# Performance work log

Hardware: AMD Instinct MI355X
Metric: run time of the kernel (lower is better)

## Reference

```python
import jax, jax.numpy as jnp
import numpy as np

EPS = 1e-07
B, C, NCON, NCC = 500000, 30, 8, 3
NH = 7  # hidden width


def _coarse_code():
    # [C, NCC] Gaussian bump coarse code, as built in __init__
    sigma = 0.25
    const_1 = 1.0 / (sigma * np.sqrt(6.28))
    ii = jnp.arange(C, dtype=jnp.float32)[:, None] / (C - 1)
    jj = jnp.arange(NCC, dtype=jnp.float32)[None, :] / (NCC - 1)
    return (const_1 * jnp.exp(-0.5 * jnp.square((ii - jj) / sigma))).astype(jnp.float32)


def _mlp(x, W1, b1, Wh, bh, Wo, bo):
    # x: [B, C, n_in]; six 7-unit ReLU layers then linear output (dropout inactive)
    h = jax.nn.relu(jnp.einsum('bci,hi->bch', x, W1) + b1)
    for i in range(Wh.shape[0]):
        h = jax.nn.relu(jnp.einsum('bci,hi->bch', h, Wh[i]) + bh[i])
    return jnp.einsum('bci,oi->bco', h, Wo) + bo


def setup_inputs() -> dict:
    key = jax.random.key(0)
    ks = jax.random.split(key, 16)
    u = lambda k, shape, lo, hi: jax.random.uniform(k, shape, jnp.float32, lo, hi)
    inp = {
        'tau': jax.random.uniform(ks[0], (B, C, NCON), jnp.float32),
        'mu_direct': jax.random.uniform(ks[1], (B, 1), jnp.float32),
        'mu_diffuse': jax.random.uniform(ks[2], (B, 1), jnp.float32),
        # net_direct: n_input = 5 + NCC + 1 = 9
        'Wd1': u(ks[3], (NH, 5 + NCC + 1), -1.0, 1.0),
        'bd1': u(ks[4], (NH,), 0.9, 1.1),
        'Wdh': u(ks[5], (5, NH, NH), -1.0, 1.0),
        'bdh': u(ks[6], (5, NH), 0.9, 1.1),
        'Wdo': u(ks[7], (3, NH), -1.0, 1.0),
        'bdo': u(ks[8], (3,), -0.1, 0.1),
        # net_diffuse: n_input = 5 + NCC = 8
        'Wf1': u(ks[9], (NH, 5 + NCC), -1.0, 1.0),
        'bf1': u(ks[10], (NH,), 0.9, 1.1),
        'Wfh': u(ks[11], (5, NH, NH), -1.0, 1.0),
        'bfh': u(ks[12], (5, NH), 0.9, 1.1),
        'Wfo': u(ks[13], (3, NH), -1.0, 1.0),
        'bfo': u(ks[14], (3,), -0.1, 0.1),
    }
    return inp


def reference(tau, mu_direct, mu_diffuse, Wd1, bd1, Wdh, bdh, Wdo, bdo,
              Wf1, bf1, Wfh, bfh, Wfo, bfo):
    tau_total = jnp.sum(tau, axis=2)                      # [B, C]
    t_direct = jnp.exp(-tau_total / (mu_direct + EPS))    # [B, C]
    t_diffuse = jnp.exp(-tau_total / (mu_diffuse + EPS))  # [B, C]

    mu_d = mu_direct[:, :, None]                          # [B, 1, 1]
    tau_direct = tau / (mu_d + EPS)                       # [B, C, NCON]

    direct_1 = (tau_direct[:, :, 3] + tau_direct[:, :, 4]
                + tau_direct[:, :, 6] + tau_direct[:, :, 7])[:, :, None]
    mu_rep = jnp.broadcast_to(mu_d, (tau.shape[0], C, 1))
    cc = jnp.broadcast_to(_coarse_code()[None], (tau.shape[0], C, NCC))

    direct = jnp.concatenate([tau_direct[:, :, 0:2], tau_direct[:, :, 5:6],
                              tau_direct[:, :, 2:3], direct_1, mu_rep, cc], axis=2)  # [B,C,9]

    diffuse_1 = (tau[:, :, 3] + tau[:, :, 4] + tau[:, :, 6] + tau[:, :, 7])[:, :, None]
    diffuse = jnp.concatenate([tau[:, :, 0:2], tau[:, :, 5:6],
                               tau[:, :, 2:3], diffuse_1, cc], axis=2)  # [B,C,8]

    e_split_direct = jax.nn.softmax(_mlp(direct, Wd1, bd1, Wdh, bdh, Wdo, bdo), axis=-1)
    e_split_diffuse = jax.nn.softmax(_mlp(diffuse, Wf1, bf1, Wfh, bfh, Wfo, bfo), axis=-1)
    return (t_direct, t_diffuse, e_split_direct, e_split_diffuse)
```

## Files before the change

### kernel.cpp

```cpp
#include <hip/hip_runtime.h>


#define B_SZ 500000
#define C_SZ 30
#define BC   (B_SZ * C_SZ)
#define EPSF 1e-7f
#define LOG2E 1.4426950408889634f

typedef float f2 __attribute__((ext_vector_type(2)));

enum {
    WD1P  = 0,
    WDHP  = 48,
    WDOP  = 328,
    BDOP  = 356,
    BEFFD = 360,
    BEFFF = 600,
    WF1P  = 840,
    WFHP  = 904,
    WFOP  = 1184,
    BFOP  = 1212,
    BDHP  = 1216,
    BFHP  = 1256,
    WS_FLOATS = 1296
};
#define FLAG_BYTE_OFF 6144

__device__ __forceinline__ float bf2f(unsigned short u) {
    union { unsigned int i; float f; } v;
    v.i = ((unsigned int)u) << 16;
    return v.f;
}

__device__ __forceinline__ unsigned short f2bf(float f) {
    union { float f; unsigned int i; } v;
    v.f = f;
    unsigned int u = v.i;
    unsigned int r = u + 0x7fffu + ((u >> 16) & 1u);
    return (unsigned short)(r >> 16);
}

__device__ __forceinline__ float ex2(float x) {
    float r;
    asm("v_exp_f32 %0, %1" : "=v"(r) : "v"(x));
    return r;
}

__device__ __forceinline__ unsigned int pk_bf16(float lo, float hi) {
    unsigned int r;
    asm("v_cvt_pk_bf16_f32 %0, %1, %2" : "=v"(r) : "v"(lo), "v"(hi));
    return r;
}

__device__ __forceinline__ f2 pkfma(f2 a, f2 b, f2 c) {
#if __has_builtin(__builtin_elementwise_fma)
    return __builtin_elementwise_fma(a, b, c);
#else
    f2 r; r.x = fmaf(a.x, b.x, c.x); r.y = fmaf(a.y, b.y, c.y); return r;
#endif
}

__device__ __forceinline__ f2 pkmax0(f2 a) {
    f2 z = {0.0f, 0.0f};
#if __has_builtin(__builtin_elementwise_max)
    return __builtin_elementwise_max(a, z);
#else
    f2 r; r.x = fmaxf(a.x, 0.f); r.y = fmaxf(a.y, 0.f); return r;
#endif
}

__device__ __forceinline__ f2 bc(f2 v, int hl) {
    return hl ? __builtin_shufflevector(v, v, 1, 1)
              : __builtin_shufflevector(v, v, 0, 0);
}

template <int NIN, int W1, int WH, int BH, int WO, int BO>
__device__ __forceinline__ void mlp_pk(const float* __restrict__ ws,
                                       const f2* __restrict__ x2,
                                       const f2* __restrict__ be,
                                       float* __restrict__ o) {
    const f2* w1 = (const f2*)(ws + W1);
    f2 h[4] = {be[0], be[1], be[2], be[3]};
#pragma unroll
    for (int i = 0; i < NIN; ++i) {
        f2 xx = bc(x2[i >> 1], i & 1);
#pragma unroll
        for (int p = 0; p < 4; ++p) h[p] = pkfma(xx, w1[i * 4 + p], h[p]);
    }
#pragma unroll
    for (int p = 0; p < 4; ++p) h[p] = pkmax0(h[p]);

    const f2* wh = (const f2*)(ws + WH);
    const f2* bh = (const f2*)(ws + BH);
#pragma unroll
    for (int l = 0; l < 5; ++l) {
        f2 hn[4];
#pragma unroll
        for (int p = 0; p < 4; ++p) hn[p] = bh[l * 4 + p];
#pragma unroll
        for (int i = 0; i < 7; ++i) {
            f2 xx = bc(h[i >> 1], i & 1);
#pragma unroll
            for (int p = 0; p < 4; ++p) hn[p] = pkfma(xx, wh[(l * 7 + i) * 4 + p], hn[p]);
        }
#pragma unroll
        for (int p = 0; p < 4; ++p) h[p] = pkmax0(hn[p]);
    }

    const f2* wo = (const f2*)(ws + WO);
    const f2* bo = (const f2*)(ws + BO);
    f2 oA = bo[0], oB = bo[1];
#pragma unroll
    for (int i = 0; i < 7; ++i) {
        f2 xx = bc(h[i >> 1], i & 1);
        oA = pkfma(xx, wo[i * 2 + 0], oA);
        oB = pkfma(xx, wo[i * 2 + 1], oB);
    }
    o[0] = oA.x; o[1] = oA.y; o[2] = oB.x;
}

struct P12 { const void* p[12]; };

__global__ void prep(P12 ptrs, const unsigned int* __restrict__ tau_raw,
                     float* __restrict__ ws, int* __restrict__ flagp)
{
    __shared__ int sflag;
    int tid = threadIdx.x;
    if (tid < 64) {
        unsigned long long m = __ballot((tau_raw[tid] & 0x8000u) != 0u);
        if (tid == 0) { sflag = (m != 0ull) ? 1 : 0; *flagp = sflag; }
    }
    __syncthreads();
    const int f32m = sflag;

    auto rd = [&](int seg, int idx) -> float {
        if (f32m) return ((const float*)ptrs.p[seg])[idx];
        return bf2f(((const unsigned short*)ptrs.p[seg])[idx]);
    };
    auto ccf = [&](int c, int k) -> float {
        const float C1 = 1.0f / (0.25f * sqrtf(6.28f));
        float ii = (float)c * (1.0f / 29.0f);
        float jj = (float)k * 0.5f;
        float d = (ii - jj) * 4.0f;
        return C1 * expf(-0.5f * d * d);
    };

    for (int i = tid; i < 48; i += 256) {
        int ii = i >> 3, p = (i >> 1) & 3, hl = i & 1, j = 2 * p + hl;
        ws[WD1P + i] = (j < 7) ? rd(0, j * 9 + ii) : 0.f;
    }
    for (int i = tid; i < 280; i += 256) {
        int l = i / 56, r = i % 56;
        int ii = r >> 3, p = (r >> 1) & 3, hl = r & 1, j = 2 * p + hl;
        ws[WDHP + i] = (j < 7) ? rd(2, l * 49 + j * 7 + ii) : 0.f;
    }
    for (int i = tid; i < 40; i += 256) {
        int l = i / 8, p = (i >> 1) & 3, hl = i & 1, j = 2 * p + hl;
        ws[BDHP + i] = (j < 7) ? rd(3, l * 7 + j) : 0.f;
    }
    for (int i = tid; i < 28; i += 256) {
        int ii = i >> 2, p = (i >> 1) & 1, hl = i & 1, k = 2 * p + hl;
        ws[WDOP + i] = (k < 3) ? rd(4, k * 7 + ii) * LOG2E : 0.f;
    }
    for (int i = tid; i < 4; i += 256)
        ws[BDOP + i] = (i < 3) ? rd(5, i) * LOG2E : 0.f;

    for (int i = tid; i < 240; i += 256) {
        int c = i / 8, j = i % 8; float v = 0.f;
        if (j < 7) v = rd(1, j) + rd(0, j * 9 + 6) * ccf(c, 0)
                               + rd(0, j * 9 + 7) * ccf(c, 1)
                               + rd(0, j * 9 + 8) * ccf(c, 2);
        ws[BEFFD + i] = v;
    }
    for (int i = tid; i < 240; i += 256) {
        int c = i / 8, j = i % 8; float v = 0.f;
        if (j < 7) v = rd(7, j) + rd(6, j * 8 + 5) * ccf(c, 0)
                               + rd(6, j * 8 + 6) * ccf(c, 1)
                               + rd(6, j * 8 + 7) * ccf(c, 2);
        ws[BEFFF + i] = v;
    }
    for (int i = tid; i < 64; i += 256) {
        int ii = i >> 3, p = (i >> 1) & 3, hl = i & 1, j = 2 * p + hl;
        const int cols[8] = {0, 1, 3, 4, 4, 2, 4, 4};
        ws[WF1P + i] = (j < 7) ? rd(6, j * 8 + cols[ii]) : 0.f;
    }
    for (int i = tid; i < 280; i += 256) {
        int l = i / 56, r = i % 56;
        int ii = r >> 3, p = (r >> 1) & 3, hl = r & 1, j = 2 * p + hl;
        ws[WFHP + i] = (j < 7) ? rd(8, l * 49 + j * 7 + ii) : 0.f;
    }
    for (int i = tid; i < 40; i += 256) {
        int l = i / 8, p = (i >> 1) & 3, hl = i & 1, j = 2 * p + hl;
        ws[BFHP + i] = (j < 7) ? rd(9, l * 7 + j) : 0.f;
    }
    for (int i = tid; i < 28; i += 256) {
        int ii = i >> 2, p = (i >> 1) & 1, hl = i & 1, k = 2 * p + hl;
        ws[WFOP + i] = (k < 3) ? rd(10, k * 7 + ii) * LOG2E : 0.f;
    }
    for (int i = tid; i < 4; i += 256)
        ws[BFOP + i] = (i < 3) ? rd(11, i) * LOG2E : 0.f;
}

__global__ __launch_bounds__(256) void scatter_main(
    const void* __restrict__ tau_p,
    const void* __restrict__ mu_dir_p,
    const void* __restrict__ mu_dif_p,
    const float* __restrict__ ws,
    const int* __restrict__ flag,
    void* __restrict__ out_p)
{
    __shared__ unsigned short sm[2048];

    int tid = threadIdx.x;
    int eb0 = blockIdx.x * 256;
    int e = eb0 + tid;
    bool act = (e < BC);
    int eL = act ? e : (BC - 1);
    int b = eL / C_SZ;
    int c = eL - b * C_SZ;
    bool tail = (eb0 + 256 > BC);

    int is_f32 = *flag;

    float t0, t1, t2, t3, t4, t5, t6, t7, mu_d, mu_f;
    if (is_f32) {
        const float4* tf = (const float4*)tau_p;
        float4 a = tf[2 * eL];
        float4 bq = tf[2 * eL + 1];
        t0 = a.x; t1 = a.y; t2 = a.z; t3 = a.w;
        t4 = bq.x; t5 = bq.y; t6 = bq.z; t7 = bq.w;
        mu_d = ((const float*)mu_dir_p)[b];
        mu_f = ((const float*)mu_dif_p)[b];
    } else {
        uint4 t = ((const uint4*)tau_p)[eL];
        t0 = bf2f((unsigned short)(t.x & 0xffffu));
        t1 = bf2f((unsigned short)(t.x >> 16));
        t2 = bf2f((unsigned short)(t.y & 0xffffu));
        t3 = bf2f((unsigned short)(t.y >> 16));
        t4 = bf2f((unsigned short)(t.z & 0xffffu));
        t5 = bf2f((unsigned short)(t.z >> 16));
        t6 = bf2f((unsigned short)(t.w & 0xffffu));
        t7 = bf2f((unsigned short)(t.w >> 16));
        mu_d = bf2f(((const unsigned short*)mu_dir_p)[b]);
        mu_f = bf2f(((const unsigned short*)mu_dif_p)[b]);
    }

    float rcp_d = __builtin_amdgcn_rcpf(mu_d + EPSF);
    float rcp_f = __builtin_amdgcn_rcpf(mu_f + EPSF);

    float tau_total = ((t0 + t1) + (t2 + t3)) + ((t4 + t5) + (t6 + t7));
    float ttl = tau_total * LOG2E;
    float t_direct  = ex2(-ttl * rcp_d);
    float t_diffuse = ex2(-ttl * rcp_f);
    float s1 = (t3 + t4) + (t6 + t7);

    f2 bed[4], bef[4];
    {
        const float4* q = (const float4*)(ws + BEFFD) + 2 * c;
        float4 qa = q[0], qb = q[1];
        bed[0] = f2{qa.x, qa.y}; bed[1] = f2{qa.z, qa.w};
        bed[2] = f2{qb.x, qb.y}; bed[3] = f2{qb.z, qb.w};
        const float4* r = (const float4*)(ws + BEFFF) + 2 * c;
        float4 ra = r[0], rb = r[1];
        bef[0] = f2{ra.x, ra.y}; bef[1] = f2{ra.z, ra.w};
        bef[2] = f2{rb.x, rb.y}; bef[3] = f2{rb.z, rb.w};
    }

    f2 xd2[3] = { f2{t0 * rcp_d, t1 * rcp_d},
                  f2{t5 * rcp_d, t2 * rcp_d},
                  f2{s1 * rcp_d, mu_d} };
    float od[3];
    mlp_pk<6, WD1P, WDHP, BDHP, WDOP, BDOP>(ws, xd2, bed, od);

    f2 xf2[4] = { f2{t0, t1}, f2{t2, t3}, f2{t4, t5}, f2{t6, t7} };
    float of_[3];
    mlp_pk<8, WF1P, WFHP, BFHP, WFOP, BFOP>(ws, xf2, bef, of_);

    float md = fmaxf(fmaxf(od[0], od[1]), od[2]);
    float d0 = ex2(od[0] - md), d1 = ex2(od[1] - md), d2 = ex2(od[2] - md);
    float rd_ = __builtin_amdgcn_rcpf(d0 + d1 + d2);
    d0 *= rd_; d1 *= rd_; d2 *= rd_;

    float mf = fmaxf(fmaxf(of_[0], of_[1]), of_[2]);
    float f0 = ex2(of_[0] - mf), f1 = ex2(of_[1] - mf), f2v = ex2(of_[2] - mf);
    float rf = __builtin_amdgcn_rcpf(f0 + f1 + f2v);
    f0 *= rf; f1 *= rf; f2v *= rf;

    if (!is_f32 && !tail) {
        unsigned int P1 = pk_bf16(t_direct, t_diffuse);
        unsigned int P2 = pk_bf16(d0, d1);
        unsigned int P3 = pk_bf16(d2, f0);
        unsigned int P4 = pk_bf16(f1, f2v);
        sm[tid]       = (unsigned short)P1;
        sm[256 + tid] = (unsigned short)(P1 >> 16);
        int db = 512 + 3 * tid;
        sm[db + 0] = (unsigned short)P2;
        sm[db + 1] = (unsigned short)(P2 >> 16);
        sm[db + 2] = (unsigned short)P3;
        int fb = 1280 + 3 * tid;
        sm[fb + 0] = (unsigned short)(P3 >> 16);
        sm[fb + 1] = (unsigned short)P4;
        sm[fb + 2] = (unsigned short)(P4 >> 16);
        __syncthreads();
        uint4 v = ((const uint4*)sm)[tid];
        unsigned int goff;
        if (tid < 32)        goff = 2u * eb0 + 16u * tid;
        else if (tid < 64)   goff = 2u * (BC + eb0) + 16u * (tid - 32);
        else if (tid < 160)  goff = 4u * BC + 6u * eb0 + 16u * (tid - 64);
        else                 goff = 10u * BC + 6u * eb0 + 16u * (tid - 160);
        *(uint4*)((char*)out_p + goff) = v;
    } else if (!is_f32) {
        if (act) {
            unsigned short* out = (unsigned short*)out_p;
            int odb = 2 * BC + 3 * e;
            int ofb = 5 * BC + 3 * e;
            out[e]       = f2bf(t_direct);
            out[BC + e]  = f2bf(t_diffuse);
            out[odb + 0] = f2bf(d0);
            out[odb + 1] = f2bf(d1);
            out[odb + 2] = f2bf(d2);
            out[ofb + 0] = f2bf(f0);
            out[ofb + 1] = f2bf(f1);
            out[ofb + 2] = f2bf(f2v);
        }
    } else {
        if (act) {
            float* out = (float*)out_p;
            int odb = 2 * BC + 3 * e;
            int ofb = 5 * BC + 3 * e;
            out[e] = t_direct;
            out[BC + e] = t_diffuse;
            out[odb + 0] = d0; out[odb + 1] = d1; out[odb + 2] = d2;
            out[ofb + 0] = f0; out[ofb + 1] = f1; out[ofb + 2] = f2v;
        }
    }
}

extern "C" void kernel_launch(void* const* d_in, const int* in_sizes, int n_in,
                              void* d_out, int out_size, void* d_ws, size_t ws_size,
                              hipStream_t stream) {
    float* ws = (float*)d_ws;
    int* flag = (int*)((char*)d_ws + FLAG_BYTE_OFF);

    P12 p;
    for (int i = 0; i < 12; ++i) p.p[i] = d_in[3 + i];
    prep<<<1, 256, 0, stream>>>(p, (const unsigned int*)d_in[0], ws, flag);

    int nblk = (BC + 255) / 256;
    scatter_main<<<nblk, 256, 0, stream>>>(
        d_in[0], d_in[1], d_in[2], ws, flag, d_out);
}
```

Before: 839.7 us.

## Process two elements per thread and share weight loads across both MLPs

Each thread now handles two elements, one from each half of the batch, and runs the direct and diffuse MLPs interleaved. Each weight load is then reused across four independent FMA chains, which also adds instruction-level parallelism. The diffuse first layer is folded from 8 inputs down to 6 by reusing the summed tau column, with the weight layout reordered to match. It also sets launch bounds for 4 blocks and halves the grid, at the cost of higher register pressure and larger shared staging.

```diff
diff --git a/kernel.cpp b/kernel.cpp
--- a/kernel.cpp
+++ b/kernel.cpp
@@ -4,6 +4,7 @@
 #define B_SZ 500000
 #define C_SZ 30
 #define BC   (B_SZ * C_SZ)
+#define HBC  (BC / 2)
 #define EPSF 1e-7f
 #define LOG2E 1.4426950408889634f
 
@@ -11,18 +12,18 @@
 
 enum {
     WD1P  = 0,
-    WDHP  = 48,
-    WDOP  = 328,
-    BDOP  = 356,
-    BEFFD = 360,
-    BEFFF = 600,
-    WF1P  = 840,
-    WFHP  = 904,
-    WFOP  = 1184,
-    BFOP  = 1212,
-    BDHP  = 1216,
-    BFHP  = 1256,
-    WS_FLOATS = 1296
+    WF1P  = 48,
+    WDHP  = 96,
+    WFHP  = 376,
+    BDHP  = 656,
+    BFHP  = 696,
+    WDOP  = 736,
+    BDOP  = 764,
+    WFOP  = 768,
+    BFOP  = 796,
+    BEFFD = 800,
+    BEFFF = 1040,
+    WS_FLOATS = 1280
 };
 #define FLAG_BYTE_OFF 6144
 
@@ -72,51 +73,6 @@
 __device__ __forceinline__ f2 bc(f2 v, int hl) {
     return hl ? __builtin_shufflevector(v, v, 1, 1)
               : __builtin_shufflevector(v, v, 0, 0);
-}
-
-template <int NIN, int W1, int WH, int BH, int WO, int BO>
-__device__ __forceinline__ void mlp_pk(const float* __restrict__ ws,
-                                       const f2* __restrict__ x2,
-                                       const f2* __restrict__ be,
-                                       float* __restrict__ o) {
-    const f2* w1 = (const f2*)(ws + W1);
-    f2 h[4] = {be[0], be[1], be[2], be[3]};
-#pragma unroll
-    for (int i = 0; i < NIN; ++i) {
-        f2 xx = bc(x2[i >> 1], i & 1);
-#pragma unroll
-        for (int p = 0; p < 4; ++p) h[p] = pkfma(xx, w1[i * 4 + p], h[p]);
-    }
-#pragma unroll
-    for (int p = 0; p < 4; ++p) h[p] = pkmax0(h[p]);
-
-    const f2* wh = (const f2*)(ws + WH);
-    const f2* bh = (const f2*)(ws + BH);
-#pragma unroll
-    for (int l = 0; l < 5; ++l) {
-        f2 hn[4];
-#pragma unroll
-        for (int p = 0; p < 4; ++p) hn[p] = bh[l * 4 + p];
-#pragma unroll
-        for (int i = 0; i < 7; ++i) {
-            f2 xx = bc(h[i >> 1], i & 1);
-#pragma unroll
-            for (int p = 0; p < 4; ++p) hn[p] = pkfma(xx, wh[(l * 7 + i) * 4 + p], hn[p]);
-        }
-#pragma unroll
-        for (int p = 0; p < 4; ++p) h[p] = pkmax0(hn[p]);
-    }
-
-    const f2* wo = (const f2*)(ws + WO);
-    const f2* bo = (const f2*)(ws + BO);
-    f2 oA = bo[0], oB = bo[1];
-#pragma unroll
-    for (int i = 0; i < 7; ++i) {
-        f2 xx = bc(h[i >> 1], i & 1);
-        oA = pkfma(xx, wo[i * 2 + 0], oA);
-        oB = pkfma(xx, wo[i * 2 + 1], oB);
-    }
-    o[0] = oA.x; o[1] = oA.y; o[2] = oB.x;
 }
 
 struct P12 { const void* p[12]; };
@@ -149,22 +105,30 @@
         int ii = i >> 3, p = (i >> 1) & 3, hl = i & 1, j = 2 * p + hl;
         ws[WD1P + i] = (j < 7) ? rd(0, j * 9 + ii) : 0.f;
     }
+    for (int i = tid; i < 48; i += 256) {
+        int ii = i >> 3, p = (i >> 1) & 3, hl = i & 1, j = 2 * p + hl;
+        ws[WF1P + i] = (j < 7 && ii < 5) ? rd(6, j * 8 + ii) : 0.f;
+    }
     for (int i = tid; i < 280; i += 256) {
         int l = i / 56, r = i % 56;
         int ii = r >> 3, p = (r >> 1) & 3, hl = r & 1, j = 2 * p + hl;
         ws[WDHP + i] = (j < 7) ? rd(2, l * 49 + j * 7 + ii) : 0.f;
+        ws[WFHP + i] = (j < 7) ? rd(8, l * 49 + j * 7 + ii) : 0.f;
     }
     for (int i = tid; i < 40; i += 256) {
         int l = i / 8, p = (i >> 1) & 3, hl = i & 1, j = 2 * p + hl;
         ws[BDHP + i] = (j < 7) ? rd(3, l * 7 + j) : 0.f;
+        ws[BFHP + i] = (j < 7) ? rd(9, l * 7 + j) : 0.f;
     }
     for (int i = tid; i < 28; i += 256) {
         int ii = i >> 2, p = (i >> 1) & 1, hl = i & 1, k = 2 * p + hl;
         ws[WDOP + i] = (k < 3) ? rd(4, k * 7 + ii) * LOG2E : 0.f;
-    }
-    for (int i = tid; i < 4; i += 256)
+        ws[WFOP + i] = (k < 3) ? rd(10, k * 7 + ii) * LOG2E : 0.f;
+    }
+    for (int i = tid; i < 4; i += 256) {
         ws[BDOP + i] = (i < 3) ? rd(5, i) * LOG2E : 0.f;
-
+        ws[BFOP + i] = (i < 3) ? rd(11, i) * LOG2E : 0.f;
+    }
     for (int i = tid; i < 240; i += 256) {
         int c = i / 8, j = i % 8; float v = 0.f;
         if (j < 7) v = rd(1, j) + rd(0, j * 9 + 6) * ccf(c, 0)
@@ -179,29 +143,9 @@
                                + rd(6, j * 8 + 7) * ccf(c, 2);
         ws[BEFFF + i] = v;
     }
-    for (int i = tid; i < 64; i += 256) {
-        int ii = i >> 3, p = (i >> 1) & 3, hl = i & 1, j = 2 * p + hl;
-        const int cols[8] = {0, 1, 3, 4, 4, 2, 4, 4};
-        ws[WF1P + i] = (j < 7) ? rd(6, j * 8 + cols[ii]) : 0.f;
-    }
-    for (int i = tid; i < 280; i += 256) {
-        int l = i / 56, r = i % 56;
-        int ii = r >> 3, p = (r >> 1) & 3, hl = r & 1, j = 2 * p + hl;
-        ws[WFHP + i] = (j < 7) ? rd(8, l * 49 + j * 7 + ii) : 0.f;
-    }
-    for (int i = tid; i < 40; i += 256) {
-        int l = i / 8, p = (i >> 1) & 3, hl = i & 1, j = 2 * p + hl;
-        ws[BFHP + i] = (j < 7) ? rd(9, l * 7 + j) : 0.f;
-    }
-    for (int i = tid; i < 28; i += 256) {
-        int ii = i >> 2, p = (i >> 1) & 1, hl = i & 1, k = 2 * p + hl;
-        ws[WFOP + i] = (k < 3) ? rd(10, k * 7 + ii) * LOG2E : 0.f;
-    }
-    for (int i = tid; i < 4; i += 256)
-        ws[BFOP + i] = (i < 3) ? rd(11, i) * LOG2E : 0.f;
-}
-
-__global__ __launch_bounds__(256) void scatter_main(
+}
+
+__global__ __launch_bounds__(256, 4) void scatter_main(
     const void* __restrict__ tau_p,
     const void* __restrict__ mu_dir_p,
     const void* __restrict__ mu_dif_p,
@@ -209,50 +153,53 @@
     const int* __restrict__ flag,
     void* __restrict__ out_p)
 {
-    __shared__ unsigned short sm[2048];
+    __shared__ unsigned short sm[2][2048];
 
     int tid = threadIdx.x;
     int eb0 = blockIdx.x * 256;
-    int e = eb0 + tid;
-    bool act = (e < BC);
-    int eL = act ? e : (BC - 1);
-    int b = eL / C_SZ;
-    int c = eL - b * C_SZ;
-    bool tail = (eb0 + 256 > BC);
+    int e0 = eb0 + tid;
+    bool act = (e0 < HBC);
+    int eL = act ? e0 : (HBC - 1);
+    int b0 = eL / C_SZ;
+    int c  = eL - b0 * C_SZ;
+    int b1 = b0 + (HBC / C_SZ);
+    bool tail = (eb0 + 256 > HBC);
 
     int is_f32 = *flag;
 
-    float t0, t1, t2, t3, t4, t5, t6, t7, mu_d, mu_f;
+    float T[2][8], MUD[2], MUF[2];
     if (is_f32) {
         const float4* tf = (const float4*)tau_p;
-        float4 a = tf[2 * eL];
-        float4 bq = tf[2 * eL + 1];
-        t0 = a.x; t1 = a.y; t2 = a.z; t3 = a.w;
-        t4 = bq.x; t5 = bq.y; t6 = bq.z; t7 = bq.w;
-        mu_d = ((const float*)mu_dir_p)[b];
-        mu_f = ((const float*)mu_dif_p)[b];
+#pragma unroll
+        for (int h = 0; h < 2; ++h) {
+            int ee = eL + h * HBC;
+            float4 a = tf[2 * ee], bq = tf[2 * ee + 1];
+            T[h][0] = a.x;  T[h][1] = a.y;  T[h][2] = a.z;  T[h][3] = a.w;
+            T[h][4] = bq.x; T[h][5] = bq.y; T[h][6] = bq.z; T[h][7] = bq.w;
+        }
+        MUD[0] = ((const float*)mu_dir_p)[b0];
+        MUD[1] = ((const float*)mu_dir_p)[b1];
+        MUF[0] = ((const float*)mu_dif_p)[b0];
+        MUF[1] = ((const float*)mu_dif_p)[b1];
     } else {
-        uint4 t = ((const uint4*)tau_p)[eL];
-        t0 = bf2f((unsigned short)(t.x & 0xffffu));
-        t1 = bf2f((unsigned short)(t.x >> 16));
-        t2 = bf2f((unsigned short)(t.y & 0xffffu));
-        t3 = bf2f((unsigned short)(t.y >> 16));
-        t4 = bf2f((unsigned short)(t.z & 0xffffu));
-        t5 = bf2f((unsigned short)(t.z >> 16));
-        t6 = bf2f((unsigned short)(t.w & 0xffffu));
-        t7 = bf2f((unsigned short)(t.w >> 16));
-        mu_d = bf2f(((const unsigned short*)mu_dir_p)[b]);
-        mu_f = bf2f(((const unsigned short*)mu_dif_p)[b]);
-    }
-
-    float rcp_d = __builtin_amdgcn_rcpf(mu_d + EPSF);
-    float rcp_f = __builtin_amdgcn_rcpf(mu_f + EPSF);
-
-    float tau_total = ((t0 + t1) + (t2 + t3)) + ((t4 + t5) + (t6 + t7));
-    float ttl = tau_total * LOG2E;
-    float t_direct  = ex2(-ttl * rcp_d);
-    float t_diffuse = ex2(-ttl * rcp_f);
-    float s1 = (t3 + t4) + (t6 + t7);
+        const uint4* tu = (const uint4*)tau_p;
+#pragma unroll
+        for (int h = 0; h < 2; ++h) {
+            uint4 t = tu[eL + h * HBC];
+            T[h][0] = bf2f((unsigned short)(t.x & 0xffffu));
+            T[h][1] = bf2f((unsigned short)(t.x >> 16));
+            T[h][2] = bf2f((unsigned short)(t.y & 0xffffu));
+            T[h][3] = bf2f((unsigned short)(t.y >> 16));
+            T[h][4] = bf2f((unsigned short)(t.z & 0xffffu));
+            T[h][5] = bf2f((unsigned short)(t.z >> 16));
+            T[h][6] = bf2f((unsigned short)(t.w & 0xffffu));
+            T[h][7] = bf2f((unsigned short)(t.w >> 16));
+        }
+        MUD[0] = bf2f(((const unsigned short*)mu_dir_p)[b0]);
+        MUD[1] = bf2f(((const unsigned short*)mu_dir_p)[b1]);
+        MUF[0] = bf2f(((const unsigned short*)mu_dif_p)[b0]);
+        MUF[1] = bf2f(((const unsigned short*)mu_dif_p)[b1]);
+    }
 
     f2 bed[4], bef[4];
     {
@@ -266,72 +213,191 @@
         bef[2] = f2{rb.x, rb.y}; bef[3] = f2{rb.z, rb.w};
     }
 
-    f2 xd2[3] = { f2{t0 * rcp_d, t1 * rcp_d},
-                  f2{t5 * rcp_d, t2 * rcp_d},
-                  f2{s1 * rcp_d, mu_d} };
-    float od[3];
-    mlp_pk<6, WD1P, WDHP, BDHP, WDOP, BDOP>(ws, xd2, bed, od);
-
-    f2 xf2[4] = { f2{t0, t1}, f2{t2, t3}, f2{t4, t5}, f2{t6, t7} };
-    float of_[3];
-    mlp_pk<8, WF1P, WFHP, BFHP, WFOP, BFOP>(ws, xf2, bef, of_);
-
-    float md = fmaxf(fmaxf(od[0], od[1]), od[2]);
-    float d0 = ex2(od[0] - md), d1 = ex2(od[1] - md), d2 = ex2(od[2] - md);
-    float rd_ = __builtin_amdgcn_rcpf(d0 + d1 + d2);
-    d0 *= rd_; d1 *= rd_; d2 *= rd_;
-
-    float mf = fmaxf(fmaxf(of_[0], of_[1]), of_[2]);
-    float f0 = ex2(of_[0] - mf), f1 = ex2(of_[1] - mf), f2v = ex2(of_[2] - mf);
-    float rf = __builtin_amdgcn_rcpf(f0 + f1 + f2v);
-    f0 *= rf; f1 *= rf; f2v *= rf;
+    float tdir[2], tdif[2];
+    f2 xd[2][3], xf[2][3];
+#pragma unroll
+    for (int h = 0; h < 2; ++h) {
+        float rcp_d = __builtin_amdgcn_rcpf(MUD[h] + EPSF);
+        float rcp_f = __builtin_amdgcn_rcpf(MUF[h] + EPSF);
+        float tt = ((T[h][0] + T[h][1]) + (T[h][2] + T[h][3]))
+                 + ((T[h][4] + T[h][5]) + (T[h][6] + T[h][7]));
+        float ttl = tt * LOG2E;
+        tdir[h] = ex2(-ttl * rcp_d);
+        tdif[h] = ex2(-ttl * rcp_f);
+        float s1 = (T[h][3] + T[h][4]) + (T[h][6] + T[h][7]);
+        xd[h][0] = f2{T[h][0] * rcp_d, T[h][1] * rcp_d};
+        xd[h][1] = f2{T[h][5] * rcp_d, T[h][2] * rcp_d};
+        xd[h][2] = f2{s1 * rcp_d, MUD[h]};
+        xf[h][0] = f2{T[h][0], T[h][1]};
+        xf[h][1] = f2{T[h][5], T[h][2]};
+        xf[h][2] = f2{s1, 0.0f};
+    }
+
+    f2 hD[2][4], hF[2][4];
+#pragma unroll
+    for (int p = 0; p < 4; ++p) {
+        hD[0][p] = bed[p]; hD[1][p] = bed[p];
+        hF[0][p] = bef[p]; hF[1][p] = bef[p];
+    }
+    {
+        const f2* w1d = (const f2*)(ws + WD1P);
+        const f2* w1f = (const f2*)(ws + WF1P);
+#pragma unroll
+        for (int i = 0; i < 6; ++i) {
+            f2 a0 = bc(xd[0][i >> 1], i & 1), a1 = bc(xd[1][i >> 1], i & 1);
+            f2 b0v = bc(xf[0][i >> 1], i & 1), b1v = bc(xf[1][i >> 1], i & 1);
+#pragma unroll
+            for (int p = 0; p < 4; ++p) {
+                f2 wd = w1d[i * 4 + p], wf = w1f[i * 4 + p];
+                hD[0][p] = pkfma(a0, wd, hD[0][p]);
+                hD[1][p] = pkfma(a1, wd, hD[1][p]);
+                hF[0][p] = pkfma(b0v, wf, hF[0][p]);
+                hF[1][p] = pkfma(b1v, wf, hF[1][p]);
+            }
+        }
+#pragma unroll
+        for (int p = 0; p < 4; ++p) {
+            hD[0][p] = pkmax0(hD[0][p]); hD[1][p] = pkmax0(hD[1][p]);
+            hF[0][p] = pkmax0(hF[0][p]); hF[1][p] = pkmax0(hF[1][p]);
+        }
+    }
+    {
+        const f2* whd = (const f2*)(ws + WDHP);
+        const f2* whf = (const f2*)(ws + WFHP);
+        const f2* bhd = (const f2*)(ws + BDHP);
+        const f2* bhf = (const f2*)(ws + BFHP);
+#pragma unroll
+        for (int l = 0; l < 5; ++l) {
+            f2 nD[2][4], nF[2][4];
+#pragma unroll
+            for (int p = 0; p < 4; ++p) {
+                f2 bd = bhd[l * 4 + p], bfv = bhf[l * 4 + p];
+                nD[0][p] = bd;  nD[1][p] = bd;
+                nF[0][p] = bfv; nF[1][p] = bfv;
+            }
+#pragma unroll
+            for (int i = 0; i < 7; ++i) {
+                f2 a0 = bc(hD[0][i >> 1], i & 1), a1 = bc(hD[1][i >> 1], i & 1);
+                f2 c0 = bc(hF[0][i >> 1], i & 1), c1 = bc(hF[1][i >> 1], i & 1);
+#pragma unroll
+                for (int p = 0; p < 4; ++p) {
+                    f2 wd = whd[(l * 7 + i) * 4 + p], wf = whf[(l * 7 + i) * 4 + p];
+                    nD[0][p] = pkfma(a0, wd, nD[0][p]);
+                    nD[1][p] = pkfma(a1, wd, nD[1][p]);
+                    nF[0][p] = pkfma(c0, wf, nF[0][p]);
+                    nF[1][p] = pkfma(c1, wf, nF[1][p]);
+                }
+            }
+#pragma unroll
+            for (int p = 0; p < 4; ++p) {
+                hD[0][p] = pkmax0(nD[0][p]); hD[1][p] = pkmax0(nD[1][p]);
+                hF[0][p] = pkmax0(nF[0][p]); hF[1][p] = pkmax0(nF[1][p]);
+            }
+        }
+    }
+    float od[2][3], of_[2][3];
+    {
+        const f2* wod = (const f2*)(ws + WDOP);
+        const f2* wof = (const f2*)(ws + WFOP);
+        const f2* bod = (const f2*)(ws + BDOP);
+        const f2* bof = (const f2*)(ws + BFOP);
+        f2 oDa[2] = {bod[0], bod[0]}, oDb[2] = {bod[1], bod[1]};
+        f2 oFa[2] = {bof[0], bof[0]}, oFb[2] = {bof[1], bof[1]};
+#pragma unroll
+        for (int i = 0; i < 7; ++i) {
+            f2 w0 = wod[i * 2 + 0], w1 = wod[i * 2 + 1];
+            f2 v0 = wof[i * 2 + 0], v1 = wof[i * 2 + 1];
+#pragma unroll
+            for (int h = 0; h < 2; ++h) {
+                f2 ad = bc(hD[h][i >> 1], i & 1);
+                f2 af = bc(hF[h][i >> 1], i & 1);
+                oDa[h] = pkfma(ad, w0, oDa[h]);
+                oDb[h] = pkfma(ad, w1, oDb[h]);
+                oFa[h] = pkfma(af, v0, oFa[h]);
+                oFb[h] = pkfma(af, v1, oFb[h]);
+            }
+        }
+#pragma unroll
+        for (int h = 0; h < 2; ++h) {
+            od[h][0] = oDa[h].x; od[h][1] = oDa[h].y; od[h][2] = oDb[h].x;
+            of_[h][0] = oFa[h].x; of_[h][1] = oFa[h].y; of_[h][2] = oFb[h].x;
+        }
+    }
+
+    float D0[2], D1[2], D2[2], F0[2], F1[2], F2[2];
+#pragma unroll
+    for (int h = 0; h < 2; ++h) {
+        float md = fmaxf(fmaxf(od[h][0], od[h][1]), od[h][2]);
+        float d0 = ex2(od[h][0] - md), d1 = ex2(od[h][1] - md), d2 = ex2(od[h][2] - md);
+        float rdd = __builtin_amdgcn_rcpf(d0 + d1 + d2);
+        D0[h] = d0 * rdd; D1[h] = d1 * rdd; D2[h] = d2 * rdd;
+        float mf = fmaxf(fmaxf(of_[h][0], of_[h][1]), of_[h][2]);
+        float f0 = ex2(of_[h][0] - mf), f1 = ex2(of_[h][1] - mf), f2v = ex2(of_[h][2] - mf);
+        float rff = __builtin_amdgcn_rcpf(f0 + f1 + f2v);
+        F0[h] = f0 * rff; F1[h] = f1 * rff; F2[h] = f2v * rff;
+    }
 
     if (!is_f32 && !tail) {
-        unsigned int P1 = pk_bf16(t_direct, t_diffuse);
-        unsigned int P2 = pk_bf16(d0, d1);
-        unsigned int P3 = pk_bf16(d2, f0);
-        unsigned int P4 = pk_bf16(f1, f2v);
-        sm[tid]       = (unsigned short)P1;
-        sm[256 + tid] = (unsigned short)(P1 >> 16);
-        int db = 512 + 3 * tid;
-        sm[db + 0] = (unsigned short)P2;
-        sm[db + 1] = (unsigned short)(P2 >> 16);
-        sm[db + 2] = (unsigned short)P3;
-        int fb = 1280 + 3 * tid;
-        sm[fb + 0] = (unsigned short)(P3 >> 16);
-        sm[fb + 1] = (unsigned short)P4;
-        sm[fb + 2] = (unsigned short)(P4 >> 16);
+#pragma unroll
+        for (int h = 0; h < 2; ++h) {
+            unsigned int P1 = pk_bf16(tdir[h], tdif[h]);
+            unsigned int P2 = pk_bf16(D0[h], D1[h]);
+            unsigned int P3 = pk_bf16(D2[h], F0[h]);
+            unsigned int P4 = pk_bf16(F1[h], F2[h]);
+            sm[h][tid]       = (unsigned short)P1;
+            sm[h][256 + tid] = (unsigned short)(P1 >> 16);
+            int db = 512 + 3 * tid;
+            sm[h][db + 0] = (unsigned short)P2;
+            sm[h][db + 1] = (unsigned short)(P2 >> 16);
+            sm[h][db + 2] = (unsigned short)P3;
+            int fb = 1280 + 3 * tid;
+            sm[h][fb + 0] = (unsigned short)(P3 >> 16);
+            sm[h][fb + 1] = (unsigned short)P4;
+            sm[h][fb + 2] = (unsigned short)(P4 >> 16);
+        }
         __syncthreads();
-        uint4 v = ((const uint4*)sm)[tid];
-        unsigned int goff;
-        if (tid < 32)        goff = 2u * eb0 + 16u * tid;
-        else if (tid < 64)   goff = 2u * (BC + eb0) + 16u * (tid - 32);
-        else if (tid < 160)  goff = 4u * BC + 6u * eb0 + 16u * (tid - 64);
-        else                 goff = 10u * BC + 6u * eb0 + 16u * (tid - 160);
-        *(uint4*)((char*)out_p + goff) = v;
+#pragma unroll
+        for (int h = 0; h < 2; ++h) {
+            uint4 v = ((const uint4*)sm[h])[tid];
+            unsigned int E = (h ? (unsigned int)HBC : 0u) + (unsigned int)eb0;
+            unsigned int goff;
+            if (tid < 32)        goff = 2u * E + 16u * tid;
+            else if (tid < 64)   goff = 2u * ((unsigned int)BC + E) + 16u * (tid - 32);
+            else if (tid < 160)  goff = 4u * (unsigned int)BC + 6u * E + 16u * (tid - 64);
+            else                 goff = 10u * (unsigned int)BC + 6u * E + 16u * (tid - 160);
+            *(uint4*)((char*)out_p + goff) = v;
+        }
     } else if (!is_f32) {
         if (act) {
             unsigned short* out = (unsigned short*)out_p;
-            int odb = 2 * BC + 3 * e;
-            int ofb = 5 * BC + 3 * e;
-            out[e]       = f2bf(t_direct);
-            out[BC + e]  = f2bf(t_diffuse);
-            out[odb + 0] = f2bf(d0);
-            out[odb + 1] = f2bf(d1);
-            out[odb + 2] = f2bf(d2);
-            out[ofb + 0] = f2bf(f0);
-            out[ofb + 1] = f2bf(f1);
-            out[ofb + 2] = f2bf(f2v);
+#pragma unroll
+            for (int h = 0; h < 2; ++h) {
+                int e = e0 + h * HBC;
+                int odb = 2 * BC + 3 * e;
+                int ofb = 5 * BC + 3 * e;
+                out[e]       = f2bf(tdir[h]);
+                out[BC + e]  = f2bf(tdif[h]);
+                out[odb + 0] = f2bf(D0[h]);
+                out[odb + 1] = f2bf(D1[h]);
+                out[odb + 2] = f2bf(D2[h]);
+                out[ofb + 0] = f2bf(F0[h]);
+                out[ofb + 1] = f2bf(F1[h]);
+                out[ofb + 2] = f2bf(F2[h]);
+            }
         }
     } else {
         if (act) {
             float* out = (float*)out_p;
-            int odb = 2 * BC + 3 * e;
-            int ofb = 5 * BC + 3 * e;
-            out[e] = t_direct;
-            out[BC + e] = t_diffuse;
-            out[odb + 0] = d0; out[odb + 1] = d1; out[odb + 2] = d2;
-            out[ofb + 0] = f0; out[ofb + 1] = f1; out[ofb + 2] = f2v;
+#pragma unroll
+            for (int h = 0; h < 2; ++h) {
+                int e = e0 + h * HBC;
+                int odb = 2 * BC + 3 * e;
+                int ofb = 5 * BC + 3 * e;
+                out[e] = tdir[h];
+                out[BC + e] = tdif[h];
+                out[odb + 0] = D0[h]; out[odb + 1] = D1[h]; out[odb + 2] = D2[h];
+                out[ofb + 0] = F0[h]; out[ofb + 1] = F1[h]; out[ofb + 2] = F2[h];
+            }
         }
     }
 }
@@ -346,7 +412,7 @@
     for (int i = 0; i < 12; ++i) p.p[i] = d_in[3 + i];
     prep<<<1, 256, 0, stream>>>(p, (const unsigned int*)d_in[0], ws, flag);
 
-    int nblk = (BC + 255) / 256;
+    int nblk = (HBC + 255) / 256;
     scatter_main<<<nblk, 256, 0, stream>>>(
         d_in[0], d_in[1], d_in[2], ws, flag, d_out);
 }
```

After: 839.1 us. About the same (-0.1%).
